# Kernel tuning notes

Measured on AMD Instinct MI355X. Metric: run time of the kernel, lower is better.

Reference implementation:

```python
import jax, jax.numpy as jnp
import numpy as np

D_MODEL, D_STATE, EXPAND = 1024, 16, 2
D_INNER = D_MODEL * EXPAND
BATCH, SEQ = 4, 2048
DT = 0.1

def setup_inputs() -> dict:
    key = jax.random.key(0)
    ks = jax.random.split(key, 12)
    s = 0.02
    inp = {
        "x": jax.random.normal(ks[0], (BATCH, SEQ, D_MODEL), jnp.float32),
        "B_mod": jax.random.normal(ks[1], (BATCH, D_STATE), jnp.float32) * 0.1,
        "C_mod": jax.random.normal(ks[2], (BATCH, D_STATE), jnp.float32) * 0.1,
        "W_in": jax.random.normal(ks[3], (D_MODEL, 2 * D_INNER), jnp.float32) * s,
        "b_in": jnp.zeros((2 * D_INNER,), jnp.float32),
        "conv_w": jax.random.normal(ks[4], (D_INNER, 1, 3), jnp.float32) * 0.3,
        "conv_b": jnp.zeros((D_INNER,), jnp.float32),
        "A_log": jnp.tile(jnp.log(jnp.arange(1, D_STATE + 1, dtype=jnp.float32))[None, :], (D_INNER, 1)),
        "D": jnp.ones((D_INNER,), jnp.float32),
        "W_B": jax.random.normal(ks[5], (D_INNER, D_STATE), jnp.float32) * s,
        "b_B": jnp.zeros((D_STATE,), jnp.float32),
        "W_C": jax.random.normal(ks[6], (D_INNER, D_STATE), jnp.float32) * s,
        "b_C": jnp.zeros((D_STATE,), jnp.float32),
        "W_out": jax.random.normal(ks[7], (D_INNER, D_MODEL), jnp.float32) * s,
        "b_out": jnp.zeros((D_MODEL,), jnp.float32),
    }
    return inp

def _silu(v):
    return v * jax.nn.sigmoid(v)

def reference(x, B_mod, C_mod, W_in, b_in, conv_w, conv_b, A_log, D, W_B, b_B, W_C, b_C, W_out, b_out):
    # in_proj + split + gate
    xr = x @ W_in + b_in                      # (B, L, 2*D_INNER)
    x_ssm, x_res = jnp.split(xr, 2, axis=-1)
    x_ssm = _silu(x_ssm)
    # depthwise conv1d, kernel 3, padding 1
    xc = jnp.transpose(x_ssm, (0, 2, 1))      # (B, C, L)
    xc = jax.lax.conv_general_dilated(
        xc, conv_w, window_strides=(1,), padding=[(1, 1)],
        dimension_numbers=("NCH", "OIH", "NCH"), feature_group_count=D_INNER)
    xc = xc + conv_b[None, :, None]
    x_ssm = jnp.transpose(xc, (0, 2, 1))      # (B, L, D_INNER)
    # SSM params
    A = -jnp.exp(A_log)                       # (D_INNER, D_STATE)
    A_bar = jnp.exp(A * DT)
    B = x_ssm @ W_B + b_B + B_mod[:, None, :] # (B, L, D_STATE)
    C = x_ssm @ W_C + b_C + C_mod[:, None, :]
    # sequential scan over time
    def step(h, inp):
        xt, Bt, Ct = inp                      # (B,D_INNER), (B,S), (B,S)
        h = A_bar[None] * h + xt[:, :, None] * Bt[:, None, :]
        yt = jnp.einsum("bds,bs->bd", h, Ct)
        return h, yt
    h0 = jnp.zeros((x.shape[0], D_INNER, D_STATE), x.dtype)
    xs = (jnp.moveaxis(x_ssm, 1, 0), jnp.moveaxis(B, 1, 0), jnp.moveaxis(C, 1, 0))
    _, ys = jax.lax.scan(step, h0, xs)        # (L, B, D_INNER)
    y = jnp.moveaxis(ys, 0, 1) + D[None, None, :] * x_ssm
    y = y * _silu(x_res)
    return y @ W_out + b_out
```

## Files before the change

kernel.cpp:

```cpp
#include <hip/hip_runtime.h>
#include <stdint.h>

#define D_MODEL 1024
#define D_STATE 16
#define D_INNER 2048
#define BATCH   4
#define SEQ     2048
#define ML      (BATCH*SEQ)
#define CH      64
#define NCHUNK  (SEQ/CH)
#define KSEG    8

typedef unsigned short u16;
typedef u16   u16x8  __attribute__((ext_vector_type(8)));
typedef short s16x8  __attribute__((ext_vector_type(8)));
typedef float f32x4  __attribute__((ext_vector_type(4)));

__device__ __forceinline__ float b2f(u16 u){
  union { uint32_t i; float f; } v; v.i = ((uint32_t)u) << 16; return v.f;
}
__device__ __forceinline__ u16 f2b(float f){
  uint32_t x = __float_as_uint(f);
  return (u16)((x + 0x7fffu + ((x >> 16) & 1u)) >> 16);
}
__device__ __forceinline__ float silu_f(float v){
  return v / (1.f + __expf(-v));
}
__device__ __forceinline__ void gl_lds16(const void* gp, void* lp){
  __builtin_amdgcn_global_load_lds(
      (const __attribute__((address_space(1))) void*)gp,
      (__attribute__((address_space(3))) void*)lp, 16, 0, 0);
}

__global__ __launch_bounds__(256) void transpose_cast_k(const float* __restrict__ in,
                                                        u16* __restrict__ out,
                                                        int R, int C){
  __shared__ float tile[32][33];
  int bx = blockIdx.x * 32, by = blockIdx.y * 32;
  int tx = threadIdx.x & 31, ty = threadIdx.x >> 5;
  #pragma unroll
  for (int i = 0; i < 32; i += 8)
    tile[ty + i][tx] = in[(size_t)(by + ty + i) * C + bx + tx];
  __syncthreads();
  #pragma unroll
  for (int i = 0; i < 32; i += 8)
    out[(size_t)(bx + ty + i) * R + by + tx] = f2b(tile[tx][ty + i]);
}

__global__ __launch_bounds__(256) void cast_k(const float* __restrict__ in,
                                              u16* __restrict__ out){
  size_t i = ((size_t)blockIdx.x * 256 + threadIdx.x) * 8;
  f32x4 a = *(const f32x4*)(in + i);
  f32x4 b = *(const f32x4*)(in + i + 4);
  u16x8 o;
  #pragma unroll
  for (int j = 0; j < 4; ++j){ o[j] = f2b(a[j]); o[4+j] = f2b(b[j]); }
  *(u16x8*)(out + i) = o;
}

__global__ __launch_bounds__(256) void bc_wt_k(const float* __restrict__ W_B,
                                               const float* __restrict__ W_C,
                                               u16* __restrict__ Wt){
  int n = blockIdx.y;
  int k = blockIdx.x * 256 + threadIdx.x;
  const float* src = (n < 16) ? W_B : W_C;
  Wt[(size_t)n * D_INNER + k] = f2b(src[(size_t)k * 16 + (n & 15)]);
}

template<int MODE>
__global__ __launch_bounds__(256) void gemm_bt(const u16* __restrict__ A,
                                               const u16* __restrict__ Bt,
                                               const float* __restrict__ bias,
                                               u16* __restrict__ out0,
                                               u16* __restrict__ out1,
                                               float* __restrict__ outf,
                                               int M, int N, int K, int n_per_xcd){
  __shared__ __align__(16) u16 Asb[2][128*32];
  __shared__ __align__(16) u16 Bsb[2][128*32];
  const int bid = blockIdx.x;
  const int xcd = bid & 7, t2 = bid >> 3;
  const int n0 = (xcd * n_per_xcd + (t2 % n_per_xcd)) * 128;
  const int m0 = (t2 / n_per_xcd) * 128;
  const int t    = threadIdx.x;
  const int wave = t >> 6, lane = t & 63;
  const int wm   = (wave >> 1) * 64, wn = (wave & 1) * 64;
  const int lrow = lane & 15, kq = (lane >> 4) * 8;
  const int srow = lane >> 2;
  const int scol = (lane & 3) * 8;

  f32x4 acc[4][4];
  #pragma unroll
  for (int i = 0; i < 4; ++i)
    #pragma unroll
    for (int j = 0; j < 4; ++j)
      acc[i][j] = (f32x4){0.f, 0.f, 0.f, 0.f};

  auto stage = [&](int buf, int k0){
    #pragma unroll
    for (int i = 0; i < 2; ++i) {
      int R0 = (wave*2 + i) * 16;
      gl_lds16(&A [(size_t)(m0 + R0 + srow)*K + k0 + scol], &Asb[buf][R0*32]);
      gl_lds16(&Bt[(size_t)(n0 + R0 + srow)*K + k0 + scol], &Bsb[buf][R0*32]);
    }
  };

  const int KT = K >> 5;
  stage(0, 0);
  __syncthreads();
  for (int kt = 0; kt < KT; ++kt) {
    const int cur = kt & 1;
    if (kt + 1 < KT) stage(1 - cur, (kt + 1) * 32);
    s16x8 af[4], bfr[4];
    #pragma unroll
    for (int i = 0; i < 4; ++i) af[i]  = *(const s16x8*)&Asb[cur][(wm + i*16 + lrow)*32 + kq];
    #pragma unroll
    for (int j = 0; j < 4; ++j) bfr[j] = *(const s16x8*)&Bsb[cur][(wn + j*16 + lrow)*32 + kq];
    #pragma unroll
    for (int i = 0; i < 4; ++i)
      #pragma unroll
      for (int j = 0; j < 4; ++j)
        acc[i][j] = __builtin_amdgcn_mfma_f32_16x16x32_bf16(af[i], bfr[j], acc[i][j], 0, 0, 0);
    __syncthreads();
  }

  const int Nh = N >> 1;
  #pragma unroll
  for (int i = 0; i < 4; ++i) {
    #pragma unroll
    for (int j = 0; j < 4; ++j) {
      int col = n0 + wn + j*16 + lrow;
      float bv = bias[col];
      #pragma unroll
      for (int r = 0; r < 4; ++r) {
        int row = m0 + wm + i*16 + (lane >> 4)*4 + r;
        float v = acc[i][j][r] + bv;
        if (MODE == 0) {
          outf[(size_t)row * N + col] = v;
        } else {
          float s = silu_f(v);
          if (col < Nh) out0[(size_t)row * Nh + col]        = f2b(s);
          else          out1[(size_t)row * Nh + (col - Nh)] = f2b(s);
        }
      }
    }
  }
}

__global__ __launch_bounds__(256) void conv_k(const u16* __restrict__ xs,
    const float* __restrict__ conv_w, const float* __restrict__ conv_b,
    u16* __restrict__ xconv){
  int bl = blockIdx.x;
  int l = bl & (SEQ-1);
  int d = threadIdx.x * 8;
  const u16* row0 = xs + (size_t)bl * D_INNER + d;

  float f0[8], fm[8], fp[8];
  { u16x8 v = *(const u16x8*)row0;
    #pragma unroll
    for (int j = 0; j < 8; ++j) f0[j] = b2f(v[j]); }
  if (l > 0) {
    u16x8 v = *(const u16x8*)(row0 - D_INNER);
    #pragma unroll
    for (int j = 0; j < 8; ++j) fm[j] = b2f(v[j]);
  } else {
    #pragma unroll
    for (int j = 0; j < 8; ++j) fm[j] = 0.f;
  }
  if (l < SEQ-1) {
    u16x8 v = *(const u16x8*)(row0 + D_INNER);
    #pragma unroll
    for (int j = 0; j < 8; ++j) fp[j] = b2f(v[j]);
  } else {
    #pragma unroll
    for (int j = 0; j < 8; ++j) fp[j] = 0.f;
  }

  const float* wp = conv_w + (size_t)d * 3;
  float wl[24];
  #pragma unroll
  for (int q = 0; q < 6; ++q){
    f32x4 v = *(const f32x4*)(wp + q*4);
    #pragma unroll
    for (int j = 0; j < 4; ++j) wl[q*4 + j] = v[j];
  }
  float cb[8];
  { f32x4 c0 = *(const f32x4*)(conv_b + d), c1 = *(const f32x4*)(conv_b + d + 4);
    #pragma unroll
    for (int j = 0; j < 4; ++j){ cb[j] = c0[j]; cb[4+j] = c1[j]; } }

  u16x8 o;
  #pragma unroll
  for (int j = 0; j < 8; ++j)
    o[j] = f2b(wl[3*j]*fm[j] + wl[3*j+1]*f0[j] + wl[3*j+2]*fp[j] + cb[j]);
  *(u16x8*)(xconv + (size_t)bl * D_INNER + d) = o;
}

__global__ __launch_bounds__(256) void bc_gemm_k(const u16* __restrict__ xconv,
                                                 const u16* __restrict__ Wt,
                                                 float* __restrict__ partial){
  __shared__ __align__(16) u16 Asb[128*40];
  __shared__ __align__(16) u16 Wsb[32*40];
  const int kseg = blockIdx.x;
  const int m0   = blockIdx.y * 128;
  const int t    = threadIdx.x;
  const int wave = t >> 6, lane = t & 63;
  const int wm   = wave * 32;
  const int lrow = lane & 15, kq = (lane >> 4) * 8;

  f32x4 acc[2][2];
  #pragma unroll
  for (int i = 0; i < 2; ++i)
    #pragma unroll
    for (int j = 0; j < 2; ++j)
      acc[i][j] = (f32x4){0.f, 0.f, 0.f, 0.f};

  const int kbase = kseg * (D_INNER / KSEG);
  for (int ks = 0; ks < (D_INNER / KSEG); ks += 32) {
    int k0 = kbase + ks;
    #pragma unroll
    for (int i = 0; i < 2; ++i) {
      int f = (i*256 + t) * 8;
      int r = f >> 5, c = f & 31;
      *(u16x8*)&Asb[r*40 + c] = *(const u16x8*)&xconv[(size_t)(m0 + r)*D_INNER + k0 + c];
    }
    if (t < 128) {
      int f = t * 8;
      int r = f >> 5, c = f & 31;
      *(u16x8*)&Wsb[r*40 + c] = *(const u16x8*)&Wt[(size_t)r*D_INNER + k0 + c];
    }
    __syncthreads();
    s16x8 af[2], wf[2];
    #pragma unroll
    for (int i = 0; i < 2; ++i) af[i] = *(const s16x8*)&Asb[(wm + i*16 + lrow)*40 + kq];
    #pragma unroll
    for (int j = 0; j < 2; ++j) wf[j] = *(const s16x8*)&Wsb[(j*16 + lrow)*40 + kq];
    #pragma unroll
    for (int i = 0; i < 2; ++i)
      #pragma unroll
      for (int j = 0; j < 2; ++j)
        acc[i][j] = __builtin_amdgcn_mfma_f32_16x16x32_bf16(af[i], wf[j], acc[i][j], 0, 0, 0);
    __syncthreads();
  }

  #pragma unroll
  for (int i = 0; i < 2; ++i)
    #pragma unroll
    for (int j = 0; j < 2; ++j)
      #pragma unroll
      for (int r = 0; r < 4; ++r) {
        int row = m0 + wm + i*16 + (lane >> 4)*4 + r;
        int col = j*16 + lrow;
        partial[((size_t)kseg * ML + row) * 32 + col] = acc[i][j][r];
      }
}

__global__ __launch_bounds__(256) void bc_reduce_k(const float* __restrict__ partial,
    const float* __restrict__ b_B, const float* __restrict__ B_mod,
    const float* __restrict__ b_C, const float* __restrict__ C_mod,
    float* __restrict__ Bbuf, float* __restrict__ Cbuf){
  int g = blockIdx.x * 256 + threadIdx.x;
  int row = g >> 5, col = g & 31;
  int b = row >> 11;
  float s = 0.f;
  #pragma unroll
  for (int seg = 0; seg < KSEG; ++seg)
    s += partial[(size_t)seg * ML * 32 + g];
  if (col < 16) Bbuf[(size_t)row*16 + col]      = s + b_B[col]      + B_mod[b*16 + col];
  else          Cbuf[(size_t)row*16 + col - 16] = s + b_C[col - 16] + C_mod[b*16 + col - 16];
}

__global__ __launch_bounds__(256) void state_k(const u16* __restrict__ xconv,
    const float* __restrict__ Bbuf, const float* __restrict__ A_log,
    float* __restrict__ hend){
  int c = blockIdx.x, db = blockIdx.y, b = blockIdx.z;
  int d = db*256 + threadIdx.x;

  float Abar[16];
  #pragma unroll
  for (int s = 0; s < 16; ++s)
    Abar[s] = __expf(-0.1f * __expf(A_log[d*16 + s]));
  float h[16];
  #pragma unroll
  for (int s = 0; s < 16; ++s) h[s] = 0.f;

  size_t base = (size_t)b * SEQ * D_INNER + (size_t)c * CH * D_INNER + d;
  const float* Br = Bbuf + ((size_t)b * SEQ + (size_t)c * CH) * 16;

  float Bc[16];
  #pragma unroll
  for (int s = 0; s < 16; ++s) Bc[s] = Br[s];
  float xn = b2f(xconv[base]);

  for (int l = 0; l < CH; ++l){
    float x = xn;
    float Bl[16];
    #pragma unroll
    for (int s = 0; s < 16; ++s) Bl[s] = Bc[s];
    if (l < CH-1){
      xn = b2f(xconv[base + (size_t)(l+1)*D_INNER]);
      #pragma unroll
      for (int s = 0; s < 16; ++s) Bc[s] = Br[(l+1)*16 + s];
    }
    #pragma unroll
    for (int s = 0; s < 16; ++s)
      h[s] = Abar[s]*h[s] + x*Bl[s];
  }
  float* hp = hend + (((size_t)(b*NCHUNK + c))*D_INNER + d)*16;
  #pragma unroll
  for (int q = 0; q < 4; ++q)
    *(f32x4*)(hp + q*4) = (f32x4){h[q*4], h[q*4+1], h[q*4+2], h[q*4+3]};
}

__global__ __launch_bounds__(256) void prefix_k(const float* __restrict__ hend,
    const float* __restrict__ A_log, float* __restrict__ hin){
  int g = blockIdx.x*256 + threadIdx.x;
  int s = g & 15;
  int d = (g >> 4) & (D_INNER-1);
  int b = g >> 15;
  float decay = __expf(-0.1f * (float)CH * __expf(A_log[d*16 + s]));
  size_t stride = (size_t)D_INNER * 16;
  const float* he = hend + (size_t)b*NCHUNK*stride + (size_t)d*16 + s;
  float*       hi = hin  + (size_t)b*NCHUNK*stride + (size_t)d*16 + s;
  float h = 0.f;
  for (int c0 = 0; c0 < NCHUNK; c0 += 8){
    float v[8];
    #pragma unroll
    for (int i = 0; i < 8; ++i) v[i] = he[(size_t)(c0+i)*stride];
    #pragma unroll
    for (int i = 0; i < 8; ++i){
      hi[(size_t)(c0+i)*stride] = h;
      h = decay*h + v[i];
    }
  }
}

__global__ __launch_bounds__(256) void scan2_k(const u16* __restrict__ xconv,
    const u16* __restrict__ gate, const float* __restrict__ Bbuf, const float* __restrict__ Cbuf,
    const float* __restrict__ A_log, const float* __restrict__ Dp,
    const float* __restrict__ hin, u16* __restrict__ ybuf){
  int c = blockIdx.x, db = blockIdx.y, b = blockIdx.z;
  int d = db*256 + threadIdx.x;

  float Abar[16];
  #pragma unroll
  for (int s = 0; s < 16; ++s)
    Abar[s] = __expf(-0.1f * __expf(A_log[d*16 + s]));
  float h[16];
  const float* hp = hin + (((size_t)(b*NCHUNK + c))*D_INNER + d)*16;
  #pragma unroll
  for (int q = 0; q < 4; ++q){
    f32x4 v = *(const f32x4*)(hp + q*4);
    #pragma unroll
    for (int j = 0; j < 4; ++j) h[q*4 + j] = v[j];
  }
  float Dd = Dp[d];

  size_t base = (size_t)b * SEQ * D_INNER + (size_t)c * CH * D_INNER + d;
  const float* Br = Bbuf + ((size_t)b * SEQ + (size_t)c * CH) * 16;
  const float* Cr = Cbuf + ((size_t)b * SEQ + (size_t)c * CH) * 16;

  float Bc[16], Cc[16];
  #pragma unroll
  for (int s = 0; s < 16; ++s){ Bc[s] = Br[s]; Cc[s] = Cr[s]; }
  float xn = b2f(xconv[base]);
  float gn = b2f(gate[base]);

  for (int l = 0; l < CH; ++l){
    float x = xn, g = gn;
    float Bl[16], Cl[16];
    #pragma unroll
    for (int s = 0; s < 16; ++s){ Bl[s] = Bc[s]; Cl[s] = Cc[s]; }
    if (l < CH-1){
      size_t idx = base + (size_t)(l+1)*D_INNER;
      xn = b2f(xconv[idx]); gn = b2f(gate[idx]);
      #pragma unroll
      for (int s = 0; s < 16; ++s){ Bc[s] = Br[(l+1)*16 + s]; Cc[s] = Cr[(l+1)*16 + s]; }
    }
    float ya[4] = {0.f, 0.f, 0.f, 0.f};
    #pragma unroll
    for (int s = 0; s < 16; ++s){
      float hv = Abar[s]*h[s] + x*Bl[s];
      h[s] = hv;
      ya[s & 3] += hv * Cl[s];
    }
    float y = ((ya[0]+ya[1]) + (ya[2]+ya[3]) + Dd*x) * g;
    ybuf[base + (size_t)l*D_INNER] = f2b(y);
  }
}

extern "C" void kernel_launch(void* const* d_in, const int* in_sizes, int n_in,
                              void* d_out, int out_size, void* d_ws, size_t ws_size,
                              hipStream_t stream){
  const float* x      = (const float*)d_in[0];
  const float* B_mod  = (const float*)d_in[1];
  const float* C_mod  = (const float*)d_in[2];
  const float* W_in   = (const float*)d_in[3];
  const float* b_in   = (const float*)d_in[4];
  const float* conv_w = (const float*)d_in[5];
  const float* conv_b = (const float*)d_in[6];
  const float* A_log  = (const float*)d_in[7];
  const float* Dp     = (const float*)d_in[8];
  const float* W_B    = (const float*)d_in[9];
  const float* b_B    = (const float*)d_in[10];
  const float* W_C    = (const float*)d_in[11];
  const float* b_C    = (const float*)d_in[12];
  const float* W_out  = (const float*)d_in[13];
  const float* b_out  = (const float*)d_in[14];
  float* out = (float*)d_out;

  char* ws = (char*)d_ws;
  size_t off = 0;
  auto alloc = [&](size_t bytes)->char* {
    char* p = ws + off; off += (bytes + 255) & ~(size_t)255; return p;
  };
  u16* Wt_in  = (u16*)alloc((size_t)(2*D_INNER)*D_MODEL*2);
  u16* Wt_out = (u16*)alloc((size_t)D_MODEL*D_INNER*2);
  u16* xs     = (u16*)alloc((size_t)ML*D_INNER*2);
  u16* gatep  = (u16*)alloc((size_t)ML*D_INNER*2);
  u16* xconv  = (u16*)alloc((size_t)ML*D_INNER*2);
  float* Bbuf = (float*)alloc((size_t)ML*D_STATE*4);
  float* Cbuf = (float*)alloc((size_t)ML*D_STATE*4);
  u16* xbf    = (u16*)alloc((size_t)ML*D_MODEL*2);
  float* hin  = (float*)alloc((size_t)BATCH*NCHUNK*D_INNER*16*4);
  u16* Wt_bc  = (u16*)alloc((size_t)32*D_INNER*2);
  float* hend    = (float*)xbf;
  float* partial = (float*)Wt_in;
  u16* ybuf = xs;

  transpose_cast_k<<<dim3((2*D_INNER)/32, D_MODEL/32), 256, 0, stream>>>(W_in, Wt_in, D_MODEL, 2*D_INNER);
  transpose_cast_k<<<dim3(D_MODEL/32, D_INNER/32),     256, 0, stream>>>(W_out, Wt_out, D_INNER, D_MODEL);
  cast_k<<<dim3((ML*D_MODEL)/(256*8)), 256, 0, stream>>>(x, xbf);
  bc_wt_k<<<dim3(D_INNER/256, 32), 256, 0, stream>>>(W_B, W_C, Wt_bc);

  gemm_bt<1><<<dim3(2048), 256, 0, stream>>>(
      xbf, Wt_in, b_in, xs, gatep, nullptr, ML, 2*D_INNER, D_MODEL, 4);

  conv_k<<<dim3(ML), 256, 0, stream>>>(xs, conv_w, conv_b, xconv);

  bc_gemm_k<<<dim3(KSEG, ML/128), 256, 0, stream>>>(xconv, Wt_bc, partial);
  bc_reduce_k<<<dim3((ML*32)/256), 256, 0, stream>>>(
      partial, b_B, B_mod, b_C, C_mod, Bbuf, Cbuf);

  state_k<<<dim3(NCHUNK, D_INNER/256, BATCH), 256, 0, stream>>>(xconv, Bbuf, A_log, hend);
  prefix_k<<<dim3((BATCH*D_INNER*16)/256), 256, 0, stream>>>(hend, A_log, hin);
  scan2_k<<<dim3(NCHUNK, D_INNER/256, BATCH), 256, 0, stream>>>(
      xconv, gatep, Bbuf, Cbuf, A_log, Dp, hin, ybuf);

  gemm_bt<0><<<dim3(512), 256, 0, stream>>>(
      ybuf, Wt_out, b_out, nullptr, nullptr, out, ML, D_MODEL, D_INNER, 1);
}
```

Baseline: 386.5 us.

## Replace in-projection GEMM with 256x256-tile, 8-wave pipelined MFMA kernel

Adds a dedicated in-projection GEMM kernel using 256x256 output tiles, 512 threads, and 64-wide K steps. Global-to-LDS loads are interleaved with four MFMA phases, separated by barriers, s_setprio, and explicit vmcnt waits, with XOR-swizzled LDS layout. Larger tiles increase data reuse per block and aim to hide load latency better. In exchange it uses heavy register pressure (128 accumulator floats plus fragments), and launches only 512 blocks, which risks occupancy and tail effects.

```diff
diff --git a/kernel.cpp b/kernel.cpp
--- a/kernel.cpp
+++ b/kernel.cpp
@@ -65,6 +65,143 @@
   int k = blockIdx.x * 256 + threadIdx.x;
   const float* src = (n < 16) ? W_B : W_C;
   Wt[(size_t)n * D_INNER + k] = f2b(src[(size_t)k * 16 + (n & 15)]);
+}
+
+#define G1_K  1024
+#define G1_NT (G1_K/64)
+
+__global__ __launch_bounds__(512, 2) void gemm1_k(const u16* __restrict__ A,
+                                                  const u16* __restrict__ Bt,
+                                                  const float* __restrict__ bias,
+                                                  u16* __restrict__ out0,
+                                                  u16* __restrict__ out1){
+  __shared__ __align__(16) u16 ldsA[4*8192];
+  __shared__ __align__(16) u16 ldsB[4*8192];
+
+  const int bid = blockIdx.x;
+  const int xcd = bid & 7, t2 = bid >> 3;
+  const int n0 = (xcd*2 + (t2 & 1)) * 256;
+  const int m0 = (t2 >> 1) * 256;
+
+  const int tid  = threadIdx.x;
+  const int wave = tid >> 6, lane = tid & 63;
+  const int wr = wave >> 2;
+  const int wc = wave & 3;
+  const int lrow = lane & 15;
+  const int q    = lane >> 4;
+  const int colu = ((q ^ ((lrow >> 1) & 3)) << 3);
+  const int srow8   = lane >> 3;
+  const int schunk8 = (((lane & 7) ^ ((lane >> 4) & 3)) << 3);
+
+  auto stageA = [&](int buf, int h, int k0){
+    const u16* s0 = A + (size_t)(m0 + h*128 + wave*16 + srow8) * G1_K + (k0 + schunk8);
+    u16* d = ldsA + (buf*2 + h)*8192 + wave*16*64;
+    gl_lds16(s0, d);
+    gl_lds16(s0 + (size_t)8*G1_K, d + 8*64);
+  };
+  auto stageB = [&](int buf, int h, int k0){
+    const u16* s0 = Bt + (size_t)(n0 + h*128 + wave*16 + srow8) * G1_K + (k0 + schunk8);
+    u16* d = ldsB + (buf*2 + h)*8192 + wave*16*64;
+    gl_lds16(s0, d);
+    gl_lds16(s0 + (size_t)8*G1_K, d + 8*64);
+  };
+
+  f32x4 acc[8][4];
+  #pragma unroll
+  for (int i = 0; i < 8; ++i)
+    #pragma unroll
+    for (int j = 0; j < 4; ++j) acc[i][j] = (f32x4){0.f,0.f,0.f,0.f};
+  s16x8 af[8][2], bfr[4][2];
+
+  stageA(0,0,0); stageB(0,0,0); stageB(0,1,0); stageA(0,1,0);
+  asm volatile("s_waitcnt vmcnt(4)" ::: "memory");
+  stageB(1,0,64); stageB(1,1,64); stageA(1,0,64);
+  asm volatile("s_waitcnt vmcnt(6)" ::: "memory");
+  __builtin_amdgcn_s_barrier();
+
+  auto mfma_pair = [&](int mi){
+    #pragma unroll
+    for (int nj = 0; nj < 4; ++nj) {
+      #pragma unroll
+      for (int kk = 0; kk < 2; ++kk) {
+        acc[mi][nj]   = __builtin_amdgcn_mfma_f32_16x16x32_bf16(af[mi][kk],   bfr[nj][kk], acc[mi][nj],   0,0,0);
+        acc[mi+1][nj] = __builtin_amdgcn_mfma_f32_16x16x32_bf16(af[mi+1][kk], bfr[nj][kk], acc[mi+1][nj], 0,0,0);
+      }
+    }
+  };
+
+  #pragma unroll 2
+  for (int tt = 0; tt < G1_NT; ++tt) {
+    const int buf = tt & 1;
+    const u16* Ab = ldsA + (buf*2 + wr)*8192 + lrow*64 + colu;
+    const u16* Bb = ldsB + (buf*2 + (wc >> 1))*8192 + ((wc & 1)*64 + lrow)*64 + colu;
+    const int k1 = (tt+1 < G1_NT ? tt+1 : G1_NT-1) * 64;
+    const int k2 = (tt+2 < G1_NT ? tt+2 : G1_NT-1) * 64;
+
+    #pragma unroll
+    for (int nj = 0; nj < 4; ++nj){
+      bfr[nj][0] = *(const s16x8*)(Bb + nj*16*64);
+      bfr[nj][1] = *(const s16x8*)(Bb + nj*16*64 + 32);
+    }
+    af[0][0] = *(const s16x8*)(Ab);
+    af[0][1] = *(const s16x8*)(Ab + 32);
+    af[1][0] = *(const s16x8*)(Ab + 16*64);
+    af[1][1] = *(const s16x8*)(Ab + 16*64 + 32);
+    stageA(buf ^ 1, 1, k1);
+    __builtin_amdgcn_s_barrier();
+    __builtin_amdgcn_s_setprio(1);
+    mfma_pair(0);
+    __builtin_amdgcn_s_setprio(0);
+    __builtin_amdgcn_s_barrier();
+
+    #pragma unroll
+    for (int i = 2; i < 5; ++i){
+      af[i][0] = *(const s16x8*)(Ab + i*16*64);
+      af[i][1] = *(const s16x8*)(Ab + i*16*64 + 32);
+    }
+    stageB(buf, 0, k2);
+    __builtin_amdgcn_s_barrier();
+    __builtin_amdgcn_s_setprio(1);
+    mfma_pair(2);
+    __builtin_amdgcn_s_setprio(0);
+    __builtin_amdgcn_s_barrier();
+
+    #pragma unroll
+    for (int i = 5; i < 8; ++i){
+      af[i][0] = *(const s16x8*)(Ab + i*16*64);
+      af[i][1] = *(const s16x8*)(Ab + i*16*64 + 32);
+    }
+    stageB(buf, 1, k2);
+    __builtin_amdgcn_s_barrier();
+    __builtin_amdgcn_s_setprio(1);
+    mfma_pair(4);
+    __builtin_amdgcn_s_setprio(0);
+    __builtin_amdgcn_s_barrier();
+
+    stageA(buf, 0, k2);
+    asm volatile("s_waitcnt vmcnt(6)" ::: "memory");
+    __builtin_amdgcn_s_barrier();
+    __builtin_amdgcn_s_setprio(1);
+    mfma_pair(6);
+    __builtin_amdgcn_s_setprio(0);
+    __builtin_amdgcn_s_barrier();
+  }
+  asm volatile("s_waitcnt vmcnt(0)" ::: "memory");
+
+  #pragma unroll
+  for (int nj = 0; nj < 4; ++nj) {
+    const int col = n0 + wc*64 + nj*16 + lrow;
+    const float bv = bias[col];
+    u16* op = (col < D_INNER) ? (out0 + col) : (out1 + (col - D_INNER));
+    #pragma unroll
+    for (int mi = 0; mi < 8; ++mi) {
+      #pragma unroll
+      for (int r = 0; r < 4; ++r) {
+        const int row = m0 + wr*128 + mi*16 + q*4 + r;
+        op[(size_t)row * D_INNER] = f2b(silu_f(acc[mi][nj][r] + bv));
+      }
+    }
+  }
 }
 
 template<int MODE>
@@ -432,8 +569,7 @@
   cast_k<<<dim3((ML*D_MODEL)/(256*8)), 256, 0, stream>>>(x, xbf);
   bc_wt_k<<<dim3(D_INNER/256, 32), 256, 0, stream>>>(W_B, W_C, Wt_bc);
 
-  gemm_bt<1><<<dim3(2048), 256, 0, stream>>>(
-      xbf, Wt_in, b_in, xs, gatep, nullptr, ML, 2*D_INNER, D_MODEL, 4);
+  gemm1_k<<<dim3(512), 512, 0, stream>>>(xbf, Wt_in, b_in, xs, gatep);
 
   conv_k<<<dim3(ML), 256, 0, stream>>>(xs, conv_w, conv_b, xconv);
 
```

New measurement: 368.8 us. -4.6%, faster.
